# Performance work log

Hardware: AMD Instinct MI355X
Metric: run time of the kernel (lower is better)

Reference implementation:

```python
import jax, jax.numpy as jnp
import numpy as np

VOCAB, TAGS, E, H, T = 100000, 50, 256, 512, 4096


def _lstm_scan(xs, W_ih, W_hh, b_ih, b_hh, reverse=False):
    # xs: [T, E]; returns hidden states [T, H]. PyTorch LSTMCell gate order: i, f, g, o.
    def step(carry, x):
        h, c = carry
        gates = x @ W_ih.T + b_ih + h @ W_hh.T + b_hh  # [4H]
        i, f, g, o = jnp.split(gates, 4)
        i, f, o = jax.nn.sigmoid(i), jax.nn.sigmoid(f), jax.nn.sigmoid(o)
        g = jnp.tanh(g)
        c_new = f * c + i * g
        h_new = o * jnp.tanh(c_new)
        return (h_new, c_new), h_new

    init = (jnp.zeros((H,), xs.dtype), jnp.zeros((H,), xs.dtype))
    _, hs = jax.lax.scan(step, init, xs, reverse=reverse)
    return hs


def setup_inputs() -> dict:
    key = jax.random.key(0)
    ks = jax.random.split(key, 12)
    s = 0.05
    return {
        "sentence": jax.random.randint(ks[0], (T,), 0, VOCAB, dtype=jnp.int32),
        "emb": jax.random.normal(ks[1], (VOCAB, E), jnp.float32) * s,
        "W_ih_f": jax.random.normal(ks[2], (4 * H, E), jnp.float32) * s,
        "W_hh_f": jax.random.normal(ks[3], (4 * H, H), jnp.float32) * s,
        "b_ih_f": jax.random.normal(ks[4], (4 * H,), jnp.float32) * s,
        "b_hh_f": jax.random.normal(ks[5], (4 * H,), jnp.float32) * s,
        "W_ih_b": jax.random.normal(ks[6], (4 * H, E), jnp.float32) * s,
        "W_hh_b": jax.random.normal(ks[7], (4 * H, H), jnp.float32) * s,
        "b_ih_b": jax.random.normal(ks[8], (4 * H,), jnp.float32) * s,
        "b_hh_b": jax.random.normal(ks[9], (4 * H,), jnp.float32) * s,
        "W_out": jax.random.normal(ks[10], (TAGS, 2 * H), jnp.float32) * s,
        "b_out": jax.random.normal(ks[11], (TAGS,), jnp.float32) * s,
    }


def reference(sentence, emb, W_ih_f, W_hh_f, b_ih_f, b_hh_f,
              W_ih_b, W_hh_b, b_ih_b, b_hh_b, W_out, b_out):
    embeds = emb[sentence]  # [T, E]
    hs_f = _lstm_scan(embeds, W_ih_f, W_hh_f, b_ih_f, b_hh_f, reverse=False)  # [T, H]
    hs_b = _lstm_scan(embeds, W_ih_b, W_hh_b, b_ih_b, b_hh_b, reverse=True)   # [T, H]
    outs = jnp.concatenate([hs_f, hs_b], axis=-1)  # [T, 2H]
    tag_space = outs @ W_out.T + b_out  # [T, TAGS]
    return tag_space[:, None, :]  # [T, 1, TAGS] to match torch.stack of [1, TAGS] rows
```

## Files before the change

kernel.cpp:

```cpp
#include <hip/hip_runtime.h>
#include <math.h>

#define T_LEN 4096
#define EDIM  256
#define HDIM  512
#define NTAGS 50
#define SENTW 0xFFFFFFFFu

__device__ __forceinline__ float sigm(float x) {
    return __builtin_amdgcn_rcpf(1.0f + __expf(-x));
}
__device__ __forceinline__ float tanh_fast(float x) {
    float e = __expf(2.0f * x);
    return 1.0f - 2.0f * __builtin_amdgcn_rcpf(e + 1.0f);
}
__device__ __forceinline__ float u2f(unsigned u) { union { unsigned i; float f; } v; v.i = u; return v.f; }
__device__ __forceinline__ float rdlane(float v, int l) {
    union { float f; int i; } a, r;
    a.f = v;
    r.i = __builtin_amdgcn_readlane(a.i, l);
    return r.f;
}
__device__ __forceinline__ unsigned long long pollA(unsigned long long* p) {
    return __hip_atomic_fetch_or(p, 0ull, __ATOMIC_RELAXED, __HIP_MEMORY_SCOPE_AGENT);
}
__device__ __forceinline__ bool bad2(unsigned long long v) {
    return ((unsigned)v == SENTW) || ((unsigned)(v >> 32) == SENTW);
}

__global__ __launch_bounds__(256, 1) void lstm_scan(
    const int* __restrict__ sent, const float* __restrict__ emb,
    const float* __restrict__ Wih_f, const float* __restrict__ Whh_f,
    const float* __restrict__ bih_f, const float* __restrict__ bhh_f,
    const float* __restrict__ Wih_b, const float* __restrict__ Whh_b,
    const float* __restrict__ bih_b, const float* __restrict__ bhh_b,
    float* hsf, float* hsb)
{
    const int tid  = threadIdx.x;
    const int lane = tid & 63;
    const int wv   = tid >> 6;
    const int dir  = blockIdx.x >> 5;
    const int g    = blockIdx.x & 31;

    const float* Wih = dir ? Wih_b : Wih_f;
    const float* Whh = dir ? Whh_b : Whh_f;
    const float* bih = dir ? bih_b : bih_f;
    const float* bhh = dir ? bhh_b : bhh_f;
    float* hs = dir ? hsb : hsf;

    const int q = lane >> 4;
    const int u = lane & 15;
    const int R = q * 512 + g * 16 + u;

    float wh[128];
    {
        const float* base = Whh + (size_t)R * HDIM + wv * 128;
        #pragma unroll
        for (int i = 0; i < 32; ++i) {
            float4 v = *(const float4*)(base + 4 * i);
            wh[4*i] = v.x; wh[4*i+1] = v.y; wh[4*i+2] = v.z; wh[4*i+3] = v.w;
        }
    }
    float wx[64];
    {
        const float* base = Wih + (size_t)R * EDIM + wv * 64;
        #pragma unroll
        for (int i = 0; i < 16; ++i) {
            float4 v = *(const float4*)(base + 4 * i);
            wx[4*i] = v.x; wx[4*i+1] = v.y; wx[4*i+2] = v.z; wx[4*i+3] = v.w;
        }
    }
    const float bias = bih[R] + bhh[R];

    __shared__ float pl[2][256];
    float c_state = 0.0f;

    float ecur;
    {
        int t0 = dir ? (T_LEN - 1) : 0;
        ecur = emb[(size_t)sent[t0] * EDIM + wv * 64 + lane];
    }

    for (int s = 0; s < T_LEN; ++s) {
        const int t = dir ? (T_LEN - 1 - s) : s;

        unsigned long long* p = nullptr;
        unsigned long long v = 0;
        if (s > 0) {
            const int tp = dir ? (t + 1) : (t - 1);
            p = (unsigned long long*)(hs + (size_t)tp * HDIM + wv * 128) + lane;
            v = pollA(p);
        }
        float enext = 0.0f;
        if (s + 1 < T_LEN) {
            int tn = dir ? (t - 1) : (t + 1);
            enext = emb[(size_t)sent[tn] * EDIM + wv * 64 + lane];
        }

        float a0 = 0.f, a1 = 0.f, a2 = 0.f, a3 = 0.f;
        #pragma unroll
        for (int i = 0; i < 16; ++i) {
            a0 = fmaf(wx[4*i+0], rdlane(ecur, 4*i+0), a0);
            a1 = fmaf(wx[4*i+1], rdlane(ecur, 4*i+1), a1);
            a2 = fmaf(wx[4*i+2], rdlane(ecur, 4*i+2), a2);
            a3 = fmaf(wx[4*i+3], rdlane(ecur, 4*i+3), a3);
        }

        if (s > 0) {
            while (bad2(v)) v = pollA(p);
            float h0 = u2f((unsigned)v);
            float h1 = u2f((unsigned)(v >> 32));
            #pragma unroll
            for (int i = 0; i < 32; ++i) {
                a0 = fmaf(wh[4*i+0], rdlane(h0, 2*i+0), a0);
                a1 = fmaf(wh[4*i+1], rdlane(h1, 2*i+0), a1);
                a2 = fmaf(wh[4*i+2], rdlane(h0, 2*i+1), a2);
                a3 = fmaf(wh[4*i+3], rdlane(h1, 2*i+1), a3);
            }
        }

        pl[s & 1][wv * 64 + lane] = (a0 + a1) + (a2 + a3);
        __syncthreads();

        if (wv == 0) {
            const float* pb = pl[s & 1];
            float tot = pb[lane] + pb[64 + lane] + pb[128 + lane] + pb[192 + lane] + bias;
            float gi = __shfl(tot, u,      64);
            float gf = __shfl(tot, u + 16, 64);
            float gg = __shfl(tot, u + 32, 64);
            float go = __shfl(tot, u + 48, 64);
            if (lane < 16) {
                float iv = sigm(gi), fv = sigm(gf);
                float gv = tanh_fast(gg), ov = sigm(go);
                c_state = fv * c_state + iv * gv;
                float h = ov * tanh_fast(c_state);
                __hip_atomic_exchange(hs + (size_t)t * HDIM + g * 16 + u, h,
                                      __ATOMIC_RELAXED, __HIP_MEMORY_SCOPE_AGENT);
            }
        }
        ecur = enext;
    }
}

__global__ __launch_bounds__(256) void out_gemm(
    const float* __restrict__ hsf, const float* __restrict__ hsb,
    const float* __restrict__ Wout, const float* __restrict__ bout,
    float* __restrict__ out)
{
    const int t   = blockIdx.x;
    const int tid = threadIdx.x;
    __shared__ float h2[1024];

    if (tid < 128)
        *(float4*)(h2 + tid * 4) = *(const float4*)(hsf + (size_t)t * HDIM + tid * 4);
    else
        *(float4*)(h2 + 512 + (tid - 128) * 4) = *(const float4*)(hsb + (size_t)t * HDIM + (tid - 128) * 4);
    __syncthreads();

    const int wv = tid >> 6, lane = tid & 63;
    for (int tag = wv; tag < NTAGS; tag += 4) {
        const float4* wr = (const float4*)(Wout + (size_t)tag * (2 * HDIM));
        float p = 0.0f;
        #pragma unroll
        for (int c = lane; c < 256; c += 64) {
            float4 wv4 = wr[c];
            float4 hv  = *(const float4*)(h2 + c * 4);
            p += wv4.x * hv.x + wv4.y * hv.y + wv4.z * hv.z + wv4.w * hv.w;
        }
        p += __shfl_down(p, 32, 64);
        p += __shfl_down(p, 16, 64);
        p += __shfl_down(p, 8, 64);
        p += __shfl_down(p, 4, 64);
        p += __shfl_down(p, 2, 64);
        p += __shfl_down(p, 1, 64);
        if (lane == 0) out[(size_t)t * NTAGS + tag] = p + bout[tag];
    }
}

extern "C" void kernel_launch(void* const* d_in, const int* in_sizes, int n_in,
                              void* d_out, int out_size, void* d_ws, size_t ws_size,
                              hipStream_t stream)
{
    const int*   sent  = (const int*)d_in[0];
    const float* emb   = (const float*)d_in[1];
    const float* Wih_f = (const float*)d_in[2];
    const float* Whh_f = (const float*)d_in[3];
    const float* bih_f = (const float*)d_in[4];
    const float* bhh_f = (const float*)d_in[5];
    const float* Wih_b = (const float*)d_in[6];
    const float* Whh_b = (const float*)d_in[7];
    const float* bih_b = (const float*)d_in[8];
    const float* bhh_b = (const float*)d_in[9];
    const float* Wout  = (const float*)d_in[10];
    const float* bout  = (const float*)d_in[11];
    float* out = (float*)d_out;

    char* ws = (char*)d_ws;
    float* hsf = (float*)(ws);
    float* hsb = (float*)(ws + 8388608);
    hipMemsetAsync(ws, 0xFF, 16777216, stream);

    lstm_scan<<<64, 256, 0, stream>>>(sent, emb,
                                      Wih_f, Whh_f, bih_f, bhh_f,
                                      Wih_b, Whh_b, bih_b, bhh_b,
                                      hsf, hsb);
    out_gemm<<<T_LEN, 256, 0, stream>>>(hsf, hsb, Wout, bout, out);
}
```

Before: 6.103 ms.

## Consume recurrent hidden state in 8-lane chunks as it arrives, prefetch poll earlier

Instead of spinning until the whole wave's 64-lane slice of the previous hidden state is valid, the recurrent dot product now proceeds in eight 8-lane chunks, each waiting only until its own lanes are ready (checked via ballot). The first poll for the next step is issued right after the block barrier, before wave 0 does the gate math. Empty asm constraints pin the weight arrays in VGPRs. This aims to overlap the cross-block wait with FMA work and hide poll latency, at the cost of extra ballot and branch overhead per chunk and an early poll that will usually see unfinished data.

```diff
diff --git a/kernel.cpp b/kernel.cpp
--- a/kernel.cpp
+++ b/kernel.cpp
@@ -70,6 +70,11 @@
             wx[4*i] = v.x; wx[4*i+1] = v.y; wx[4*i+2] = v.z; wx[4*i+3] = v.w;
         }
     }
+    #pragma unroll
+    for (int i = 0; i < 128; ++i) asm volatile("" : "+v"(wh[i]));
+    #pragma unroll
+    for (int i = 0; i < 64; ++i)  asm volatile("" : "+v"(wx[i]));
+
     const float bias = bih[R] + bhh[R];
 
     __shared__ float pl[2][256];
@@ -81,16 +86,12 @@
         ecur = emb[(size_t)sent[t0] * EDIM + wv * 64 + lane];
     }
 
+    unsigned long long* p = nullptr;
+    unsigned long long  v = 0;
+
     for (int s = 0; s < T_LEN; ++s) {
         const int t = dir ? (T_LEN - 1 - s) : s;
 
-        unsigned long long* p = nullptr;
-        unsigned long long v = 0;
-        if (s > 0) {
-            const int tp = dir ? (t + 1) : (t - 1);
-            p = (unsigned long long*)(hs + (size_t)tp * HDIM + wv * 128) + lane;
-            v = pollA(p);
-        }
         float enext = 0.0f;
         if (s + 1 < T_LEN) {
             int tn = dir ? (t - 1) : (t + 1);
@@ -107,20 +108,39 @@
         }
 
         if (s > 0) {
-            while (bad2(v)) v = pollA(p);
-            float h0 = u2f((unsigned)v);
-            float h1 = u2f((unsigned)(v >> 32));
+            unsigned long long rdy = __ballot(!bad2(v));
             #pragma unroll
-            for (int i = 0; i < 32; ++i) {
-                a0 = fmaf(wh[4*i+0], rdlane(h0, 2*i+0), a0);
-                a1 = fmaf(wh[4*i+1], rdlane(h1, 2*i+0), a1);
-                a2 = fmaf(wh[4*i+2], rdlane(h0, 2*i+1), a2);
-                a3 = fmaf(wh[4*i+3], rdlane(h1, 2*i+1), a3);
+            for (int j = 0; j < 8; ++j) {
+                const unsigned long long m = 0xFFull << (8 * j);
+                while ((rdy & m) != m) {
+                    if (bad2(v)) v = pollA(p);
+                    rdy = __ballot(!bad2(v));
+                }
+                float h0 = u2f((unsigned)v);
+                float h1 = u2f((unsigned)(v >> 32));
+                #pragma unroll
+                for (int e = 0; e < 8; ++e) {
+                    const int ln = 8 * j + e;
+                    if ((e & 1) == 0) {
+                        a0 = fmaf(wh[16*j + 2*e],     rdlane(h0, ln), a0);
+                        a1 = fmaf(wh[16*j + 2*e + 1], rdlane(h1, ln), a1);
+                    } else {
+                        a2 = fmaf(wh[16*j + 2*e],     rdlane(h0, ln), a2);
+                        a3 = fmaf(wh[16*j + 2*e + 1], rdlane(h1, ln), a3);
+                    }
+                }
             }
         }
 
         pl[s & 1][wv * 64 + lane] = (a0 + a1) + (a2 + a3);
         __syncthreads();
+
+        unsigned long long* pn = nullptr;
+        unsigned long long  vn = 0;
+        if (s + 1 < T_LEN) {
+            pn = (unsigned long long*)(hs + (size_t)t * HDIM + wv * 128) + lane;
+            vn = pollA(pn);
+        }
 
         if (wv == 0) {
             const float* pb = pl[s & 1];
@@ -138,6 +158,7 @@
                                       __ATOMIC_RELAXED, __HIP_MEMORY_SCOPE_AGENT);
             }
         }
+        p = pn; v = vn;
         ecur = enext;
     }
 }
```

Result: slower. 8.543 ms (+40.0%).

## Split LSTM gate epilogue across all four waves and pre-issue next-step h poll

Applied to the files above, without the earlier changes.

Instead of wave 0 alone reducing the four partial sums and computing all 16 hidden units, every wave now reduces its own slice of the partials with xor-shuffles and computes four units, with biases folded into per-lane registers. The shared partial buffer gets a padded stride to avoid bank conflicts. The atomic poll for the next step's hidden state is issued right after the barrier, so its latency overlaps the gate math. This shortens the serial critical path of each recurrent step, at the cost of extra shuffles in every wave and earlier polling that may spin more.

```diff
diff --git a/kernel.cpp b/kernel.cpp
--- a/kernel.cpp
+++ b/kernel.cpp
@@ -70,9 +70,16 @@
             wx[4*i] = v.x; wx[4*i+1] = v.y; wx[4*i+2] = v.z; wx[4*i+3] = v.w;
         }
     }
-    const float bias = bih[R] + bhh[R];
-
-    __shared__ float pl[2][256];
+    float bi = 0.f, bff = 0.f, bgg = 0.f, boo = 0.f;
+    if (lane < 4) {
+        int uu = g * 16 + wv * 4 + lane;
+        bi  = bih[uu]        + bhh[uu];
+        bff = bih[512 + uu]  + bhh[512 + uu];
+        bgg = bih[1024 + uu] + bhh[1024 + uu];
+        boo = bih[1536 + uu] + bhh[1536 + uu];
+    }
+
+    __shared__ float pl[2][284];
     float c_state = 0.0f;
 
     float ecur;
@@ -81,16 +88,12 @@
         ecur = emb[(size_t)sent[t0] * EDIM + wv * 64 + lane];
     }
 
+    unsigned long long* p = nullptr;
+    unsigned long long  v = 0;
+
     for (int s = 0; s < T_LEN; ++s) {
         const int t = dir ? (T_LEN - 1 - s) : s;
 
-        unsigned long long* p = nullptr;
-        unsigned long long v = 0;
-        if (s > 0) {
-            const int tp = dir ? (t + 1) : (t - 1);
-            p = (unsigned long long*)(hs + (size_t)tp * HDIM + wv * 128) + lane;
-            v = pollA(p);
-        }
         float enext = 0.0f;
         if (s + 1 < T_LEN) {
             int tn = dir ? (t - 1) : (t + 1);
@@ -119,22 +122,32 @@
             }
         }
 
-        pl[s & 1][wv * 64 + lane] = (a0 + a1) + (a2 + a3);
+        pl[s & 1][wv * 71 + lane] = (a0 + a1) + (a2 + a3);
         __syncthreads();
 
-        if (wv == 0) {
-            const float* pb = pl[s & 1];
-            float tot = pb[lane] + pb[64 + lane] + pb[128 + lane] + pb[192 + lane] + bias;
-            float gi = __shfl(tot, u,      64);
-            float gf = __shfl(tot, u + 16, 64);
-            float gg = __shfl(tot, u + 32, 64);
-            float go = __shfl(tot, u + 48, 64);
-            if (lane < 16) {
-                float iv = sigm(gi), fv = sigm(gf);
-                float gv = tanh_fast(gg), ov = sigm(go);
+        if (s + 1 < T_LEN) {
+            p = (unsigned long long*)(hs + (size_t)t * HDIM + wv * 128) + lane;
+            v = pollA(p);
+        }
+
+        {
+            const int sw = lane >> 4;
+            const int qq = (lane >> 2) & 3;
+            const int m  = lane & 3;
+            float val = pl[s & 1][sw * 71 + qq * 16 + wv * 4 + m];
+            val += __shfl_xor(val, 16, 64);
+            val += __shfl_xor(val, 32, 64);
+            const int m2 = lane & 3;
+            float gi = __shfl(val, m2,      64);
+            float gf = __shfl(val, 4 + m2,  64);
+            float gg = __shfl(val, 8 + m2,  64);
+            float go = __shfl(val, 12 + m2, 64);
+            if (lane < 4) {
+                float iv = sigm(gi + bi), fv = sigm(gf + bff);
+                float gv = tanh_fast(gg + bgg), ov = sigm(go + boo);
                 c_state = fv * c_state + iv * gv;
                 float h = ov * tanh_fast(c_state);
-                __hip_atomic_exchange(hs + (size_t)t * HDIM + g * 16 + u, h,
+                __hip_atomic_exchange(hs + (size_t)t * HDIM + g * 16 + wv * 4 + lane, h,
                                       __ATOMIC_RELAXED, __HIP_MEMORY_SCOPE_AGENT);
             }
         }
```

Result: slower. 7.251 ms (+18.8%).
